# Kernel optimization log

Measured on AMD Instinct MI355X. Metric: run time of the kernel, lower is better.

The kernel has to match this reference:

```python
import jax, jax.numpy as jnp
import numpy as np

N_NODES = 100000
N_EDGES = 1600000
IN_C, HID_C, OUT_C = 128, 128, 64


def gcn_conv(x, src, dst, ew, W, b, n_nodes):
    """PyG GCNConv: symmetric-normalized aggregation with added self-loops.

    out = D^{-1/2} (A + I) D^{-1/2} (x @ W) + b,  D = deg(A+I)
    """
    h = x @ W  # [N, C_out]
    # degree at target nodes, including self-loop weight of 1
    deg = jax.ops.segment_sum(ew, dst, num_segments=n_nodes) + 1.0  # [N]
    dinv = jnp.where(deg > 0, jax.lax.rsqrt(deg), 0.0)
    norm = dinv[src] * ew * dinv[dst]  # [E]
    # gather-scale-scatter over edges + self-loop term (norm_ii = 1/deg_i)
    agg = jax.ops.segment_sum(h[src] * norm[:, None], dst, num_segments=n_nodes)
    agg = agg + h * (dinv * dinv)[:, None]
    return agg + b


def setup_inputs() -> dict:
    key = jax.random.key(0)
    ks = jax.random.split(key, 7)
    x = jax.random.normal(ks[0], (N_NODES, IN_C), dtype=jnp.float32)
    edge_index = jax.random.randint(ks[1], (2, N_EDGES), 0, N_NODES, dtype=jnp.int32)
    edge_weight = jax.random.uniform(ks[2], (N_EDGES,), dtype=jnp.float32)
    W1 = jax.random.normal(ks[3], (IN_C, HID_C), dtype=jnp.float32) / np.sqrt(IN_C)
    b1 = jnp.zeros((HID_C,), dtype=jnp.float32)
    W2 = jax.random.normal(ks[4], (HID_C, OUT_C), dtype=jnp.float32) / np.sqrt(HID_C)
    b2 = jnp.zeros((OUT_C,), dtype=jnp.float32)
    return {"x": x, "edge_index": edge_index, "edge_weight": edge_weight,
            "W1": W1, "b1": b1, "W2": W2, "b2": b2}


def reference(x, edge_index, edge_weight, W1, b1, W2, b2):
    src, dst = edge_index[0], edge_index[1]
    n = x.shape[0]
    h = gcn_conv(x, src, dst, edge_weight, W1, b1, n)
    h = jax.nn.relu(h)
    out = gcn_conv(h, src, dst, edge_weight, W2, b2, n)
    return out
```

## Files before the change

### kernel.cpp

```cpp
#include <hip/hip_runtime.h>


#define N_NODES 100000
#define CHUNK   2048
#define NBUCK   196
#define BSHIFT  9
#define BNODES  512
#define CAP     10240

__device__ __forceinline__ unsigned bf16r(float f) {
    unsigned u = __float_as_uint(f);
    return (u + 0x7fffu + ((u >> 16) & 1u)) >> 16;
}
__device__ __forceinline__ float bf_lo(unsigned u) { return __uint_as_float(u << 16); }
__device__ __forceinline__ float bf_hi(unsigned u) { return __uint_as_float(u & 0xffff0000u); }


__global__ __launch_bounds__(256) void partA1_kernel(
    const int* __restrict__ dst, int* __restrict__ histmat, int E)
{
    __shared__ int hist[256];
    int t = threadIdx.x, blk = blockIdx.x;
    hist[t] = 0;
    __syncthreads();
    int e0 = blk * CHUNK;
    int nv = min(CHUNK, E - e0);
#pragma unroll
    for (int j = 0; j < CHUNK / 256; ++j) {
        int idx = t + j * 256;
        if (idx < nv) atomicAdd(&hist[dst[e0 + idx] >> BSHIFT], 1);
    }
    __syncthreads();
    histmat[blk * 256 + t] = hist[t];
}


__global__ __launch_bounds__(256) void scanB_kernel(
    int* __restrict__ histmat, int* __restrict__ bucketSize, int NBLK)
{
    __shared__ int sums[256];
    int b = blockIdx.x, t = threadIdx.x;
    const int PER = (NBLK + 255) / 256;
    int loc[8];
    int s = 0;
#pragma unroll 8
    for (int j = 0; j < PER; ++j) {
        int r = t * PER + j;
        int v = (r < NBLK) ? histmat[r * 256 + b] : 0;
        loc[j] = v; s += v;
    }
    sums[t] = s;
    __syncthreads();
    int v = s;
#pragma unroll
    for (int off = 1; off < 256; off <<= 1) {
        int a = (t >= off) ? sums[t - off] : 0;
        __syncthreads();
        sums[t] += a;
        __syncthreads();
    }
    if (t == 255) bucketSize[b] = sums[255];
    int run = sums[t] - v;
#pragma unroll 8
    for (int j = 0; j < PER; ++j) {
        int r = t * PER + j;
        if (r < NBLK) { histmat[r * 256 + b] = run; run += loc[j]; }
    }
}


__global__ __launch_bounds__(256) void partA2_kernel(
    const int* __restrict__ src, const int* __restrict__ dst,
    const float* __restrict__ ew, const int* __restrict__ histmat,
    uint2* __restrict__ csrTmp, int E)
{
    __shared__ int hist[256], sc[256], exc[256], lcur[256], basel[256];
    __shared__ uint2 ent[CHUNK];
    __shared__ unsigned short bof[CHUNK];

    int t = threadIdx.x, blk = blockIdx.x;
    hist[t] = 0; lcur[t] = 0;
    basel[t] = histmat[blk * 256 + t];
    __syncthreads();

    int e0 = blk * CHUNK;
    int nv = min(CHUNK, E - e0);
    int dv[CHUNK / 256]; int sv[CHUNK / 256]; unsigned wv[CHUNK / 256];
#pragma unroll
    for (int j = 0; j < CHUNK / 256; ++j) {
        int idx = t + j * 256;
        if (idx < nv) {
            int e = e0 + idx;
            dv[j] = dst[e]; sv[j] = src[e]; wv[j] = __float_as_uint(ew[e]);
            atomicAdd(&hist[dv[j] >> BSHIFT], 1);
        } else dv[j] = -1;
    }
    __syncthreads();
    int hv = hist[t];
    sc[t] = hv;
    __syncthreads();
#pragma unroll
    for (int off = 1; off < 256; off <<= 1) {
        int a = (t >= off) ? sc[t - off] : 0;
        __syncthreads();
        sc[t] += a;
        __syncthreads();
    }
    exc[t] = sc[t] - hv;
    __syncthreads();
#pragma unroll
    for (int j = 0; j < CHUNK / 256; ++j) {
        if (dv[j] >= 0) {
            int b  = dv[j] >> BSHIFT;
            int dl = dv[j] & (BNODES - 1);
            int p  = exc[b] + atomicAdd(&lcur[b], 1);
            ent[p] = make_uint2(((unsigned)dl << 17) | (unsigned)sv[j], wv[j]);
            bof[p] = (unsigned short)b;
        }
    }
    __syncthreads();
#pragma unroll
    for (int j = 0; j < CHUNK / 256; ++j) {
        int i = t + j * 256;
        if (i < nv) {
            int b = bof[i];
            size_t addr = (size_t)b * CAP + basel[b] + (i - exc[b]);
            csrTmp[addr] = ent[i];
        }
    }
}


__global__ __launch_bounds__(1024) void bucketB1_kernel(
    const uint2* __restrict__ csrTmp, const int* __restrict__ bucketSize,
    float* __restrict__ dinv, uint2* __restrict__ nodeinfo, int N)
{
    __shared__ unsigned long long dc[BNODES];
    __shared__ int scn[BNODES];
    int b = blockIdx.x, t = threadIdx.x;
    if (t < BNODES) dc[t] = 0ull;
    __syncthreads();

    int sz = bucketSize[b];
    const uint2* reg = csrTmp + (size_t)b * CAP;
    for (int i = t; i < sz; i += 1024) {
        uint2 en = reg[i];
        int dl = (int)(en.x >> 17);
        unsigned fx = (unsigned)__float2uint_rn(__uint_as_float(en.y) * 16777216.0f);
        atomicAdd(&dc[dl], (1ull << 32) | (unsigned long long)fx);
    }
    __syncthreads();

    int cnt = 0; float dv = 1.0f;
    if (t < BNODES) {
        unsigned long long v = dc[t];
        cnt = (int)(v >> 32);
        float deg = (float)(unsigned)(v & 0xffffffffull) * (1.0f / 16777216.0f);
        dv = rsqrtf(deg + 1.0f);
        scn[t] = cnt;
    }
    __syncthreads();
#pragma unroll
    for (int off = 1; off < BNODES; off <<= 1) {
        int a = 0;
        if (t < BNODES && t >= off) a = scn[t - off];
        __syncthreads();
        if (t < BNODES) scn[t] += a;
        __syncthreads();
    }
    if (t < BNODES) {
        int excl = scn[t] - cnt;
        int gn = b * BNODES + t;
        if (gn < N) {
            dinv[gn] = dv;
            nodeinfo[gn] = make_uint2((unsigned)(b * CAP + excl), (unsigned)cnt);
        }
    }
}


__global__ __launch_bounds__(1024) void bucketB2_kernel(
    const uint2* __restrict__ csrTmp, const int* __restrict__ bucketSize,
    const uint2* __restrict__ nodeinfo, const float* __restrict__ dinv,
    uint2* __restrict__ csrF, int N)
{
    __shared__ float dinv_l[BNODES];
    __shared__ int beg[BNODES], cur[BNODES];
    int b = blockIdx.x, t = threadIdx.x;
    if (t < BNODES) {
        int gn = b * BNODES + t;
        float dv = 1.0f; int bg = 0;
        if (gn < N) { uint2 inf = nodeinfo[gn]; bg = (int)inf.x; dv = dinv[gn]; }
        dinv_l[t] = dv; beg[t] = bg; cur[t] = 0;
    }
    __syncthreads();

    int sz = bucketSize[b];
    const uint2* reg = csrTmp + (size_t)b * CAP;
    for (int i = t; i < sz; i += 1024) {
        uint2 en = reg[i];
        int dl = (int)(en.x >> 17);
        int s  = (int)(en.x & 0x1FFFFu);
        int p  = beg[dl] + atomicAdd(&cur[dl], 1);
        float w = dinv[s] * __uint_as_float(en.y) * dinv_l[dl];
        csrF[p] = make_uint2((unsigned)s, __float_as_uint(w));
    }
}


template <int NCOL>
__global__ __launch_bounds__(256) void gemm_kernel(
    const float* __restrict__ X, const float* __restrict__ W,
    unsigned* __restrict__ Hb, int M)
{
    constexpr int K    = 128;
    constexpr int KT   = 32;
    constexpr int ROWS = 64;
    constexpr int GX   = NCOL / 2;
    constexpr int NG   = 256 / GX;
    constexpr int RPT  = ROWS / NG;

    __shared__ float sX[ROWS][KT + 4];
    __shared__ float sW[KT][NCOL];

    const int tid   = threadIdx.x;
    const int tx    = tid % GX;
    const int tg    = tid / GX;
    const int rbase = blockIdx.x * ROWS;

    float acc[RPT][2];
#pragma unroll
    for (int r = 0; r < RPT; ++r) { acc[r][0] = 0.f; acc[r][1] = 0.f; }

    for (int kb = 0; kb < K; kb += KT) {
#pragma unroll
        for (int it = 0; it < (ROWS * KT / 4) / 256; ++it) {
            int fq  = tid + it * 256;
            int row = fq / (KT / 4);
            int kc  = fq % (KT / 4);
            int gr  = rbase + row;
            float4 v = make_float4(0.f, 0.f, 0.f, 0.f);
            if (gr < M) v = *(const float4*)&X[(size_t)gr * K + kb + kc * 4];
            *(float4*)&sX[row][kc * 4] = v;
        }
#pragma unroll
        for (int it = 0; it < (KT * NCOL / 4) / 256; ++it) {
            int fq = tid + it * 256;
            int k  = fq / (NCOL / 4);
            int c  = fq % (NCOL / 4);
            *(float4*)&sW[k][c * 4] = *(const float4*)&W[(size_t)(kb + k) * NCOL + c * 4];
        }
        __syncthreads();

#pragma unroll
        for (int kc = 0; kc < KT; kc += 4) {
            float2 w0 = *(float2*)&sW[kc + 0][2 * tx];
            float2 w1 = *(float2*)&sW[kc + 1][2 * tx];
            float2 w2 = *(float2*)&sW[kc + 2][2 * tx];
            float2 w3 = *(float2*)&sW[kc + 3][2 * tx];
#pragma unroll
            for (int r = 0; r < RPT; ++r) {
                float4 xv = *(float4*)&sX[tg * RPT + r][kc];
                acc[r][0] = fmaf(xv.x, w0.x, acc[r][0]);
                acc[r][1] = fmaf(xv.x, w0.y, acc[r][1]);
                acc[r][0] = fmaf(xv.y, w1.x, acc[r][0]);
                acc[r][1] = fmaf(xv.y, w1.y, acc[r][1]);
                acc[r][0] = fmaf(xv.z, w2.x, acc[r][0]);
                acc[r][1] = fmaf(xv.z, w2.y, acc[r][1]);
                acc[r][0] = fmaf(xv.w, w3.x, acc[r][0]);
                acc[r][1] = fmaf(xv.w, w3.y, acc[r][1]);
            }
        }
        __syncthreads();
    }

#pragma unroll
    for (int r = 0; r < RPT; ++r) {
        int gr = rbase + tg * RPT + r;
        if (gr < M) {
            unsigned pack = bf16r(acc[r][0]) | (bf16r(acc[r][1]) << 16);
            Hb[(size_t)gr * GX + tx] = pack;
        }
    }
}


template <bool RELU>
__global__ __launch_bounds__(256) void gather128_kernel(
    const uint2* __restrict__ nodeinfo, const uint2* __restrict__ csr,
    const uint4* __restrict__ Hb4,
    const float* __restrict__ dinv, const float* __restrict__ bias,
    float* __restrict__ OUT, int N)
{
    int node = blockIdx.x * 4 + (threadIdx.x >> 6);
    if (node >= N) return;
    int lane = threadIdx.x & 63;
    int q  = lane >> 4;
    int cg = lane & 15;

    float d2; { float di = dinv[node]; d2 = (q == 0) ? di * di : 0.f; }
    float acc[8];
    {
        uint4 su = Hb4[(size_t)node * 16 + cg];
        acc[0] = bf_lo(su.x) * d2; acc[1] = bf_hi(su.x) * d2;
        acc[2] = bf_lo(su.y) * d2; acc[3] = bf_hi(su.y) * d2;
        acc[4] = bf_lo(su.z) * d2; acc[5] = bf_hi(su.z) * d2;
        acc[6] = bf_lo(su.w) * d2; acc[7] = bf_hi(su.w) * d2;
    }

    uint2 inf = nodeinfo[node];
    int beg = (int)inf.x, end = beg + (int)inf.y;
    for (int j = beg; j < end; j += 64) {
        int cs = 0, cw = 0;
        if (j + lane < end) {
            uint2 p = csr[j + lane];
            cs = (int)p.x; cw = (int)p.y;
        }
        int mm = end - j; if (mm > 64) mm = 64;
#pragma unroll 4
        for (int k = 0; k < mm; k += 4) {
            int   idx = k + q;
            int   s = __shfl(cs, idx);
            float w = __uint_as_float(__shfl(cw, idx));
            uint4 u = Hb4[(size_t)s * 16 + cg];
            acc[0] = fmaf(bf_lo(u.x), w, acc[0]); acc[1] = fmaf(bf_hi(u.x), w, acc[1]);
            acc[2] = fmaf(bf_lo(u.y), w, acc[2]); acc[3] = fmaf(bf_hi(u.y), w, acc[3]);
            acc[4] = fmaf(bf_lo(u.z), w, acc[4]); acc[5] = fmaf(bf_hi(u.z), w, acc[5]);
            acc[6] = fmaf(bf_lo(u.w), w, acc[6]); acc[7] = fmaf(bf_hi(u.w), w, acc[7]);
        }
    }

#pragma unroll
    for (int v = 0; v < 8; ++v) {
        acc[v] += __shfl_xor(acc[v], 16);
        acc[v] += __shfl_xor(acc[v], 32);
    }

    int c = cg * 8 + q * 2;
    float o0 = acc[q * 2]     + bias[c];
    float o1 = acc[q * 2 + 1] + bias[c + 1];
    if (RELU) { o0 = fmaxf(o0, 0.f); o1 = fmaxf(o1, 0.f); }
    *(float2*)&OUT[(size_t)node * 128 + c] = make_float2(o0, o1);
}


template <bool RELU>
__global__ __launch_bounds__(256) void gather64_kernel(
    const uint2* __restrict__ nodeinfo, const uint2* __restrict__ csr,
    const uint4* __restrict__ Hb4,
    const float* __restrict__ dinv, const float* __restrict__ bias,
    float* __restrict__ OUT, int N)
{
    int node = blockIdx.x * 4 + (threadIdx.x >> 6);
    if (node >= N) return;
    int lane = threadIdx.x & 63;
    int q  = lane >> 3;
    int cg = lane & 7;

    float d2; { float di = dinv[node]; d2 = (q == 0) ? di * di : 0.f; }
    float acc[8];
    {
        uint4 su = Hb4[(size_t)node * 8 + cg];
        acc[0] = bf_lo(su.x) * d2; acc[1] = bf_hi(su.x) * d2;
        acc[2] = bf_lo(su.y) * d2; acc[3] = bf_hi(su.y) * d2;
        acc[4] = bf_lo(su.z) * d2; acc[5] = bf_hi(su.z) * d2;
        acc[6] = bf_lo(su.w) * d2; acc[7] = bf_hi(su.w) * d2;
    }

    uint2 inf = nodeinfo[node];
    int beg = (int)inf.x, end = beg + (int)inf.y;
    for (int j = beg; j < end; j += 64) {
        int cs = 0, cw = 0;
        if (j + lane < end) {
            uint2 p = csr[j + lane];
            cs = (int)p.x; cw = (int)p.y;
        }
        int mm = end - j; if (mm > 64) mm = 64;
#pragma unroll 2
        for (int k = 0; k < mm; k += 8) {
            int   idx = k + q;
            int   s = __shfl(cs, idx);
            float w = __uint_as_float(__shfl(cw, idx));
            uint4 u = Hb4[(size_t)s * 8 + cg];
            acc[0] = fmaf(bf_lo(u.x), w, acc[0]); acc[1] = fmaf(bf_hi(u.x), w, acc[1]);
            acc[2] = fmaf(bf_lo(u.y), w, acc[2]); acc[3] = fmaf(bf_hi(u.y), w, acc[3]);
            acc[4] = fmaf(bf_lo(u.z), w, acc[4]); acc[5] = fmaf(bf_hi(u.z), w, acc[5]);
            acc[6] = fmaf(bf_lo(u.w), w, acc[6]); acc[7] = fmaf(bf_hi(u.w), w, acc[7]);
        }
    }

#pragma unroll
    for (int v = 0; v < 8; ++v) {
        acc[v] += __shfl_xor(acc[v], 8);
        acc[v] += __shfl_xor(acc[v], 16);
        acc[v] += __shfl_xor(acc[v], 32);
    }

    int c = cg * 8 + q;
    float o = acc[q] + bias[c];
    if (RELU) o = fmaxf(o, 0.f);
    OUT[(size_t)node * 64 + c] = o;
}

static inline size_t align_up(size_t x) { return (x + 255) & ~size_t(255); }

extern "C" void kernel_launch(void* const* d_in, const int* in_sizes, int n_in,
                              void* d_out, int out_size, void* d_ws, size_t ws_size,
                              hipStream_t stream)
{
    const float* x  = (const float*)d_in[0];
    const int*   ei = (const int*)d_in[1];
    const float* ew = (const float*)d_in[2];
    const float* W1 = (const float*)d_in[3];
    const float* b1 = (const float*)d_in[4];
    const float* W2 = (const float*)d_in[5];
    const float* b2 = (const float*)d_in[6];
    float* out = (float*)d_out;

    const int N = N_NODES;
    const int E = in_sizes[2];
    const int* src = ei;
    const int* dst = ei + E;

    const int NBLK = (E + CHUNK - 1) / CHUNK;
    const size_t REGION = (size_t)NBUCK * CAP;

    char* ws = (char*)d_ws;
    int*   histmat   = (int*)ws;   ws += align_up((size_t)NBLK * 256 * 4);
    int*   bucketSize= (int*)ws;   ws += align_up((size_t)NBUCK * 4);
    float* dinv      = (float*)ws; ws += align_up((size_t)N * 4);
    uint2* nodeinfo  = (uint2*)ws; ws += align_up((size_t)N * 8);
    uint2* csrTmp    = (uint2*)ws; ws += align_up(REGION * 8);
    uint2* csrF      = (uint2*)ws; ws += align_up(REGION * 8);
    unsigned* h1     = (unsigned*)ws; ws += align_up((size_t)N * 128 * 2);
    float*    g1     = (float*)ws;    ws += align_up((size_t)N * 128 * 4);
    unsigned* h2     = (unsigned*)ws; ws += align_up((size_t)N * 64 * 2);

    partA1_kernel<<<NBLK, 256, 0, stream>>>(dst, histmat, E);
    scanB_kernel<<<NBUCK, 256, 0, stream>>>(histmat, bucketSize, NBLK);
    partA2_kernel<<<NBLK, 256, 0, stream>>>(src, dst, ew, histmat, csrTmp, E);
    bucketB1_kernel<<<NBUCK, 1024, 0, stream>>>(csrTmp, bucketSize, dinv, nodeinfo, N);
    bucketB2_kernel<<<NBUCK, 1024, 0, stream>>>(csrTmp, bucketSize, nodeinfo, dinv, csrF, N);

    gemm_kernel<128><<<(N + 63) / 64, 256, 0, stream>>>(x, W1, h1, N);
    gather128_kernel<true><<<(N + 3) / 4, 256, 0, stream>>>(
        nodeinfo, csrF, (const uint4*)h1, dinv, b1, g1, N);

    gemm_kernel<64><<<(N + 63) / 64, 256, 0, stream>>>(g1, W2, h2, N);
    gather64_kernel<false><<<(N + 3) / 4, 256, 0, stream>>>(
        nodeinfo, csrF, (const uint4*)h2, dinv, b2, out, N);
}
```

Baseline: 339.9 us.

## Use bf16 MFMA GEMMs and store layer-1 activations as bf16

Replaces the scalar FP32 FMA GEMM kernels with bf16 MFMA 16x16x32 kernels. Weights are pre-packed into a transposed bf16 layout by a small prep kernel, and the X tile is converted to bf16 in shared memory. The first gather now writes its ReLU output as packed bf16 instead of fp32, which halves the intermediate traffic and lets the second GEMM load bf16 directly. This cuts GEMM compute cost and memory bandwidth at the cost of reduced input precision in both GEMMs.

```diff
diff --git a/kernel.cpp b/kernel.cpp
--- a/kernel.cpp
+++ b/kernel.cpp
@@ -7,6 +7,9 @@
 #define BSHIFT  9
 #define BNODES  512
 #define CAP     10240
+
+typedef __attribute__((ext_vector_type(8))) short bf16x8;
+typedef __attribute__((ext_vector_type(4))) float f32x4;
 
 __device__ __forceinline__ unsigned bf16r(float f) {
     unsigned u = __float_as_uint(f);
@@ -208,89 +211,123 @@
 }
 
 
-template <int NCOL>
-__global__ __launch_bounds__(256) void gemm_kernel(
-    const float* __restrict__ X, const float* __restrict__ W,
+__global__ __launch_bounds__(256) void prep_w_kernel(
+    const float* __restrict__ W1, const float* __restrict__ W2,
+    unsigned* __restrict__ Wt1, unsigned* __restrict__ Wt2)
+{
+    int t = threadIdx.x;
+    if (blockIdx.x == 0) {
+        for (int f = t; f < 128 * 64; f += 256) {
+            int c = f % 128, j = f / 128;
+            unsigned p = bf16r(W1[(size_t)(2 * j) * 128 + c]) |
+                         (bf16r(W1[(size_t)(2 * j + 1) * 128 + c]) << 16);
+            Wt1[c * 64 + j] = p;
+        }
+    } else {
+        for (int f = t; f < 64 * 64; f += 256) {
+            int c = f % 64, j = f / 64;
+            unsigned p = bf16r(W2[(size_t)(2 * j) * 64 + c]) |
+                         (bf16r(W2[(size_t)(2 * j + 1) * 64 + c]) << 16);
+            Wt2[c * 64 + j] = p;
+        }
+    }
+}
+
+
+template <int NCOL, bool XBF16>
+__global__ __launch_bounds__(256) void gemm_mfma_kernel(
+    const void* __restrict__ Xv, const unsigned* __restrict__ Wt,
     unsigned* __restrict__ Hb, int M)
 {
-    constexpr int K    = 128;
-    constexpr int KT   = 32;
-    constexpr int ROWS = 64;
-    constexpr int GX   = NCOL / 2;
-    constexpr int NG   = 256 / GX;
-    constexpr int RPT  = ROWS / NG;
-
-    __shared__ float sX[ROWS][KT + 4];
-    __shared__ float sW[KT][NCOL];
-
-    const int tid   = threadIdx.x;
-    const int tx    = tid % GX;
-    const int tg    = tid / GX;
-    const int rbase = blockIdx.x * ROWS;
-
-    float acc[RPT][2];
-#pragma unroll
-    for (int r = 0; r < RPT; ++r) { acc[r][0] = 0.f; acc[r][1] = 0.f; }
-
-    for (int kb = 0; kb < K; kb += KT) {
-#pragma unroll
-        for (int it = 0; it < (ROWS * KT / 4) / 256; ++it) {
-            int fq  = tid + it * 256;
-            int row = fq / (KT / 4);
-            int kc  = fq % (KT / 4);
-            int gr  = rbase + row;
+    constexpr int KU  = 64;
+    constexpr int LW  = KU + 4;
+    constexpr int NT  = (NCOL == 128) ? 2 : 1;
+    __shared__ unsigned sA[64 * LW];
+    __shared__ unsigned sB[NCOL * LW];
+
+    const int t = threadIdx.x;
+    const int rbase = blockIdx.x * 64;
+
+    for (int f = t; f < NCOL * (KU / 4); f += 256) {
+        int c = f / (KU / 4), q = f % (KU / 4);
+        uint4 v = *(const uint4*)&Wt[c * KU + q * 4];
+        *(uint4*)&sB[c * LW + q * 4] = v;
+    }
+    if (XBF16) {
+        const unsigned* Xu = (const unsigned*)Xv;
+        for (int f = t; f < 64 * (KU / 4); f += 256) {
+            int r = f / (KU / 4), q = f % (KU / 4);
+            int gr = rbase + r;
+            uint4 v = make_uint4(0, 0, 0, 0);
+            if (gr < M) v = *(const uint4*)&Xu[(size_t)gr * KU + q * 4];
+            *(uint4*)&sA[r * LW + q * 4] = v;
+        }
+    } else {
+        const float* Xf = (const float*)Xv;
+        for (int f = t; f < 64 * 32; f += 256) {
+            int r = f / 32, c4 = f % 32;
+            int gr = rbase + r;
             float4 v = make_float4(0.f, 0.f, 0.f, 0.f);
-            if (gr < M) v = *(const float4*)&X[(size_t)gr * K + kb + kc * 4];
-            *(float4*)&sX[row][kc * 4] = v;
-        }
-#pragma unroll
-        for (int it = 0; it < (KT * NCOL / 4) / 256; ++it) {
-            int fq = tid + it * 256;
-            int k  = fq / (NCOL / 4);
-            int c  = fq % (NCOL / 4);
-            *(float4*)&sW[k][c * 4] = *(const float4*)&W[(size_t)(kb + k) * NCOL + c * 4];
-        }
-        __syncthreads();
-
-#pragma unroll
-        for (int kc = 0; kc < KT; kc += 4) {
-            float2 w0 = *(float2*)&sW[kc + 0][2 * tx];
-            float2 w1 = *(float2*)&sW[kc + 1][2 * tx];
-            float2 w2 = *(float2*)&sW[kc + 2][2 * tx];
-            float2 w3 = *(float2*)&sW[kc + 3][2 * tx];
-#pragma unroll
-            for (int r = 0; r < RPT; ++r) {
-                float4 xv = *(float4*)&sX[tg * RPT + r][kc];
-                acc[r][0] = fmaf(xv.x, w0.x, acc[r][0]);
-                acc[r][1] = fmaf(xv.x, w0.y, acc[r][1]);
-                acc[r][0] = fmaf(xv.y, w1.x, acc[r][0]);
-                acc[r][1] = fmaf(xv.y, w1.y, acc[r][1]);
-                acc[r][0] = fmaf(xv.z, w2.x, acc[r][0]);
-                acc[r][1] = fmaf(xv.z, w2.y, acc[r][1]);
-                acc[r][0] = fmaf(xv.w, w3.x, acc[r][0]);
-                acc[r][1] = fmaf(xv.w, w3.y, acc[r][1]);
-            }
-        }
-        __syncthreads();
-    }
-
-#pragma unroll
-    for (int r = 0; r < RPT; ++r) {
-        int gr = rbase + tg * RPT + r;
-        if (gr < M) {
-            unsigned pack = bf16r(acc[r][0]) | (bf16r(acc[r][1]) << 16);
-            Hb[(size_t)gr * GX + tx] = pack;
-        }
-    }
-}
-
-
-template <bool RELU>
+            if (gr < M) v = *(const float4*)&Xf[(size_t)gr * 128 + c4 * 4];
+            sA[r * LW + c4 * 2]     = bf16r(v.x) | (bf16r(v.y) << 16);
+            sA[r * LW + c4 * 2 + 1] = bf16r(v.z) | (bf16r(v.w) << 16);
+        }
+    }
+    __syncthreads();
+
+    const int wave = t >> 6, lane = t & 63;
+    const int quad = lane >> 4, lr = lane & 15;
+    const int n0 = wave * (16 * NT);
+
+    f32x4 acc[4][NT];
+#pragma unroll
+    for (int mi = 0; mi < 4; ++mi)
+#pragma unroll
+        for (int ni = 0; ni < NT; ++ni)
+            acc[mi][ni] = (f32x4){0.f, 0.f, 0.f, 0.f};
+
+#pragma unroll
+    for (int ks = 0; ks < 4; ++ks) {
+        int ko = ks * 16 + quad * 4;
+        bf16x8 b[NT];
+#pragma unroll
+        for (int ni = 0; ni < NT; ++ni)
+            b[ni] = *(const bf16x8*)&sB[(n0 + ni * 16 + lr) * LW + ko];
+#pragma unroll
+        for (int mi = 0; mi < 4; ++mi) {
+            bf16x8 a = *(const bf16x8*)&sA[(mi * 16 + lr) * LW + ko];
+#pragma unroll
+            for (int ni = 0; ni < NT; ++ni)
+                acc[mi][ni] = __builtin_amdgcn_mfma_f32_16x16x32_bf16(
+                    a, b[ni], acc[mi][ni], 0, 0, 0);
+        }
+    }
+    __syncthreads();
+
+    unsigned short* sO = (unsigned short*)sA;
+#pragma unroll
+    for (int mi = 0; mi < 4; ++mi)
+#pragma unroll
+        for (int ni = 0; ni < NT; ++ni)
+#pragma unroll
+            for (int r = 0; r < 4; ++r)
+                sO[(mi * 16 + quad * 4 + r) * (2 * LW) + n0 + ni * 16 + lr] =
+                    (unsigned short)bf16r(acc[mi][ni][r]);
+    __syncthreads();
+
+    for (int f = t; f < 64 * (NCOL / 2); f += 256) {
+        int row = f / (NCOL / 2), cu = f % (NCOL / 2);
+        int gr = rbase + row;
+        if (gr < M) Hb[(size_t)gr * (NCOL / 2) + cu] = sA[row * LW + cu];
+    }
+}
+
+
 __global__ __launch_bounds__(256) void gather128_kernel(
     const uint2* __restrict__ nodeinfo, const uint2* __restrict__ csr,
     const uint4* __restrict__ Hb4,
     const float* __restrict__ dinv, const float* __restrict__ bias,
-    float* __restrict__ OUT, int N)
+    unsigned* __restrict__ OUTP, int N)
 {
     int node = blockIdx.x * 4 + (threadIdx.x >> 6);
     if (node >= N) return;
@@ -337,14 +374,12 @@
     }
 
     int c = cg * 8 + q * 2;
-    float o0 = acc[q * 2]     + bias[c];
-    float o1 = acc[q * 2 + 1] + bias[c + 1];
-    if (RELU) { o0 = fmaxf(o0, 0.f); o1 = fmaxf(o1, 0.f); }
-    *(float2*)&OUT[(size_t)node * 128 + c] = make_float2(o0, o1);
-}
-
-
-template <bool RELU>
+    float o0 = fmaxf(acc[q * 2]     + bias[c],     0.f);
+    float o1 = fmaxf(acc[q * 2 + 1] + bias[c + 1], 0.f);
+    OUTP[(size_t)node * 64 + cg * 4 + q] = bf16r(o0) | (bf16r(o1) << 16);
+}
+
+
 __global__ __launch_bounds__(256) void gather64_kernel(
     const uint2* __restrict__ nodeinfo, const uint2* __restrict__ csr,
     const uint4* __restrict__ Hb4,
@@ -397,9 +432,7 @@
     }
 
     int c = cg * 8 + q;
-    float o = acc[q] + bias[c];
-    if (RELU) o = fmaxf(o, 0.f);
-    OUT[(size_t)node * 64 + c] = o;
+    OUT[(size_t)node * 64 + c] = acc[q] + bias[c];
 }
 
 static inline size_t align_up(size_t x) { return (x + 255) & ~size_t(255); }
@@ -432,21 +465,24 @@
     uint2* nodeinfo  = (uint2*)ws; ws += align_up((size_t)N * 8);
     uint2* csrTmp    = (uint2*)ws; ws += align_up(REGION * 8);
     uint2* csrF      = (uint2*)ws; ws += align_up(REGION * 8);
-    unsigned* h1     = (unsigned*)ws; ws += align_up((size_t)N * 128 * 2);
-    float*    g1     = (float*)ws;    ws += align_up((size_t)N * 128 * 4);
-    unsigned* h2     = (unsigned*)ws; ws += align_up((size_t)N * 64 * 2);
-
+    unsigned* Wt1    = (unsigned*)ws; ws += align_up((size_t)128 * 64 * 4);
+    unsigned* Wt2    = (unsigned*)ws; ws += align_up((size_t)64 * 64 * 4);
+    unsigned* h1     = (unsigned*)ws; ws += align_up((size_t)N * 64 * 4);
+    unsigned* g1     = (unsigned*)ws; ws += align_up((size_t)N * 64 * 4);
+    unsigned* h2     = (unsigned*)ws; ws += align_up((size_t)N * 32 * 4);
+
+    prep_w_kernel<<<2, 256, 0, stream>>>(W1, W2, Wt1, Wt2);
     partA1_kernel<<<NBLK, 256, 0, stream>>>(dst, histmat, E);
     scanB_kernel<<<NBUCK, 256, 0, stream>>>(histmat, bucketSize, NBLK);
     partA2_kernel<<<NBLK, 256, 0, stream>>>(src, dst, ew, histmat, csrTmp, E);
     bucketB1_kernel<<<NBUCK, 1024, 0, stream>>>(csrTmp, bucketSize, dinv, nodeinfo, N);
     bucketB2_kernel<<<NBUCK, 1024, 0, stream>>>(csrTmp, bucketSize, nodeinfo, dinv, csrF, N);
 
-    gemm_kernel<128><<<(N + 63) / 64, 256, 0, stream>>>(x, W1, h1, N);
-    gather128_kernel<true><<<(N + 3) / 4, 256, 0, stream>>>(
+    gemm_mfma_kernel<128, false><<<(N + 63) / 64, 256, 0, stream>>>(x, Wt1, h1, N);
+    gather128_kernel<<<(N + 3) / 4, 256, 0, stream>>>(
         nodeinfo, csrF, (const uint4*)h1, dinv, b1, g1, N);
 
-    gemm_kernel<64><<<(N + 63) / 64, 256, 0, stream>>>(g1, W2, h2, N);
-    gather64_kernel<false><<<(N + 3) / 4, 256, 0, stream>>>(
+    gemm_mfma_kernel<64, true><<<(N + 63) / 64, 256, 0, stream>>>(g1, Wt2, h2, N);
+    gather64_kernel<<<(N + 3) / 4, 256, 0, stream>>>(
         nodeinfo, csrF, (const uint4*)h2, dinv, b2, out, N);
 }
```

Measured after the change: 297.4 us. 1.14x faster.
